# Performance work log

Hardware: AMD Instinct MI355X
Metric: run time of the kernel (lower is better)

## Reference

```python
import jax, jax.numpy as jnp
from jax import lax
import numpy as np

DIM = 768      # model dim
NL = 12        # num mamba layers
DS = 16        # d_state
DI = 1536      # d_inner = 2*dim
DC = 4         # d_conv
P = 16         # patch size
IMG = 256
NP = (IMG // P) ** 2  # 256 patches
GS = 5         # KAN grid_size
SO = 3         # KAN spline_order
NK = NL // 3   # 4 KAN layers
BATCH = 32


def setup_inputs() -> dict:
    key = jax.random.key(0)
    ks = jax.random.split(key, 16)
    def n(k, shape, s=0.02):
        return jax.random.normal(k, shape, jnp.float32) * s
    return {
        "x": jax.random.normal(ks[0], (BATCH, 3, IMG, IMG), jnp.float32),
        "patch_w": n(ks[1], (DIM, 3, P, P)),
        "patch_b": jnp.zeros((DIM,), jnp.float32),
        "pos_embed": n(ks[2], (1, NP, DIM)),
        "in_proj_w": n(ks[3], (NL, 2 * DI, DIM)),
        "conv_w": n(ks[4], (NL, DI, 1, DC), 0.1),
        "conv_b": jnp.zeros((NL, DI), jnp.float32),
        "x_proj_w": n(ks[5], (NL, 2 * DS, DI)),
        "dt_proj_w": n(ks[6], (NL, DS, DI)),
        "dt_proj_b": jnp.zeros((NL, DS), jnp.float32),
        "A_log": jnp.tile(jnp.log(jnp.arange(1, DS + 1, dtype=jnp.float32)), (NL, 1)),
        "D_param": jnp.ones((NL, DI), jnp.float32),
        "out_proj_w": n(ks[7], (NL, DIM, DI)),
        "kan_base_w": n(ks[8], (NK, DIM, DIM)),
        "kan_coeff": n(ks[9], (NK, DIM, DIM, GS + SO), 0.1),
        "kan_bias": n(ks[10], (NK, DIM), 0.01),
        "norm_w": jnp.ones((DIM,), jnp.float32),
        "norm_b": jnp.zeros((DIM,), jnp.float32),
    }


def _mamba_block(x, in_w, cw, cb, xpw, dtw, dtb, alog, Dp, ow):
    Bsz, L, _ = x.shape
    xr = jnp.einsum('bld,ed->ble', x, in_w)              # [B,L,2*DI]
    x1, res = xr[..., :DI], xr[..., DI:]
    # causal depthwise conv (pad d_conv-1 on left, truncate to L)
    xc = lax.conv_general_dilated(
        x1.transpose(0, 2, 1), cw, (1,), [(DC - 1, 0)],
        feature_group_count=DI,
        dimension_numbers=('NCH', 'OIH', 'NCH')) + cb[None, :, None]
    x1 = jax.nn.silu(xc.transpose(0, 2, 1))              # [B,L,DI]
    x_dbl = jnp.einsum('bld,ed->ble', x1, xpw)           # [B,L,2*DS]
    Bp = x_dbl[..., DS:]                                 # dt half of x_proj is discarded (as in torch)
    dt = jax.nn.softplus(jnp.einsum('bld,nd->bln', x1, dtw) + dtb)  # [B,L,DS]
    A = -jnp.exp(alog)                                   # [DS]
    Ad = jnp.exp(A * dt)                                 # [B,L,DS]
    u = x1[..., :DI // DS].mean(-1)                      # [B,L]
    Bd = dt * Bp * u[..., None]                          # [B,L,DS]
    def step(s, ab):
        a, b = ab
        s = s * a + b
        return s, s
    _, ys = lax.scan(step, jnp.zeros((Bsz, DS), x.dtype),
                     (Ad.transpose(1, 0, 2), Bd.transpose(1, 0, 2)))
    y = ys.transpose(1, 0, 2)                            # [B,L,DS]
    y = jnp.repeat(y, DI // DS, axis=-1)                 # n -> (n d)
    y = y + x1 * Dp
    y = y * jax.nn.silu(res)
    return jnp.einsum('bld,ed->ble', y, ow)              # [B,L,DIM]


def _kan(xf, bw, coeff, bias):
    base = xf @ bw.T + bias
    grid = jnp.linspace(-1.0, 1.0, GS + 1)
    denom = grid[1:] - grid[:-1] + 1e-8
    xs = (xf[..., None] - grid[:-1]) / denom             # [M,DIM,GS]
    basis = jnp.where((xs >= 0) & (xs < 1), xs, 0.0)
    return base + jnp.einsum('bik,oik->bo', basis, coeff[:, :, :GS])


def reference(x, patch_w, patch_b, pos_embed, in_proj_w, conv_w, conv_b,
              x_proj_w, dt_proj_w, dt_proj_b, A_log, D_param, out_proj_w,
              kan_base_w, kan_coeff, kan_bias, norm_w, norm_b):
    Bsz = x.shape[0]
    h = lax.conv_general_dilated(
        x, patch_w, (P, P), 'VALID',
        dimension_numbers=('NCHW', 'OIHW', 'NCHW')) + patch_b[None, :, None, None]
    h = h.transpose(0, 2, 3, 1).reshape(Bsz, NP, DIM) + pos_embed
    for i in range(NL):
        h = _mamba_block(h, in_proj_w[i], conv_w[i], conv_b[i], x_proj_w[i],
                         dt_proj_w[i], dt_proj_b[i], A_log[i], D_param[i], out_proj_w[i])
        if i % 3 == 2 and i // 3 < NK:
            j = i // 3
            hf = h.reshape(-1, DIM)
            h = _kan(hf, kan_base_w[j], kan_coeff[j], kan_bias[j]).reshape(Bsz, NP, DIM) + h
    mu = h.mean(-1, keepdims=True)
    var = ((h - mu) ** 2).mean(-1, keepdims=True)
    return (h - mu) / jnp.sqrt(var + 1e-5) * norm_w + norm_b
```

## Files before the change

### kernel.cpp

```cpp
#include <hip/hip_runtime.h>

#define BATCH 32
#define NPATCH 256
#define MROWS (BATCH * NPATCH)
#define DIM 768
#define DI 1536
#define DS 16

typedef __bf16 bf16_t;
typedef __attribute__((ext_vector_type(8))) __bf16 bf16x8;
typedef __attribute__((ext_vector_type(4))) float floatx4;

__device__ __forceinline__ float bf2f(unsigned short u) {
    union { unsigned int i; float f; } v; v.i = ((unsigned int)u) << 16; return v.f;
}
__device__ __forceinline__ unsigned short f2bf(float f) {
    union { float f; unsigned int i; } u; u.f = f;
    unsigned int r = u.i + 0x7FFFu + ((u.i >> 16) & 1u);
    return (unsigned short)(r >> 16);
}
__device__ __forceinline__ float ldin(const void* p, int i, int bf) {
    if (bf) return bf2f(((const unsigned short*)p)[i]);
    return ((const float*)p)[i];
}
__device__ __forceinline__ float4 ldin4(const void* p, int i, int bf) {
    if (bf) {
        ushort4 u = *(const ushort4*)((const unsigned short*)p + i);
        return make_float4(bf2f(u.x), bf2f(u.y), bf2f(u.z), bf2f(u.w));
    }
    return *(const float4*)((const float*)p + i);
}
__device__ __forceinline__ float siluf(float x) { return x / (1.0f + expf(-x)); }

__global__ void detect_k(const void* alog, int* flag) {
    if (threadIdx.x == 0 && blockIdx.x == 0) {
        float v = ((const float*)alog)[1];
        flag[0] = (fabsf(v - 0.69314718f) < 0.01f) ? 0 : 1;
    }
}

__global__ __launch_bounds__(256) void cvt4_k(const int* __restrict__ flag,
                                              const void* __restrict__ in,
                                              unsigned short* __restrict__ out, int n4) {
    int i = blockIdx.x * 256 + threadIdx.x;
    if (i >= n4) return;
    float4 v = ldin4(in, i * 4, flag[0]);
    ushort4 o;
    o.x = f2bf(v.x); o.y = f2bf(v.y); o.z = f2bf(v.z); o.w = f2bf(v.w);
    *(ushort4*)(out + i * 4) = o;
}

__global__ __launch_bounds__(256) void kcoef_k(const int* __restrict__ flag,
                                               const void* __restrict__ co,
                                               bf16_t* __restrict__ out) {
    int idx = blockIdx.x * 256 + threadIdx.x;
    int bf = flag[0];
    int j = idx / (768 * 3840);
    int r = idx - j * (768 * 3840);
    int n = r / 3840;
    int kk = r - n * 3840;
    int i = kk / 5, k5 = kk - i * 5;
    out[idx] = (bf16_t)ldin(co, ((j * 768 + n) * 768 + i) * 8 + k5, bf);
}

__global__ __launch_bounds__(256) void wproj_k(const int* __restrict__ flag,
                                               const void* __restrict__ dtw,
                                               const void* __restrict__ xpw,
                                               bf16_t* __restrict__ w2) {
    int idx = blockIdx.x * 256 + threadIdx.x;
    int bf = flag[0];
    int i = idx / (128 * 1536);
    int r = idx - i * (128 * 1536);
    int n = r / 1536, k = r - n * 1536;
    float v;
    if (n < 16)       v = ldin(dtw, (i * 16 + n) * 1536 + k, bf);
    else if (n < 32)  v = ldin(xpw, (i * 32 + n) * 1536 + k, bf);
    else if (n == 32) v = (k < 96) ? (1.0f / 96.0f) : 0.0f;
    else              v = 0.0f;
    w2[idx] = (bf16_t)v;
}

__global__ __launch_bounds__(256) void cvtconv_k(const int* __restrict__ flag,
                                                 const void* __restrict__ cw,
                                                 bf16_t* __restrict__ cwr) {
    int idx = blockIdx.x * 256 + threadIdx.x;
    int bf = flag[0];
    int i = idx / (4 * 1536);
    int r = idx - i * (4 * 1536);
    int k = r / 1536, c = r - k * 1536;
    cwr[idx] = (bf16_t)ldin(cw, i * 1536 * 4 + c * 4 + k, bf);
}

__global__ __launch_bounds__(256) void basis_k(const bf16_t* __restrict__ h,
                                               bf16_t* __restrict__ bas) {
    int idx = blockIdx.x * 256 + threadIdx.x;
    int m = idx / 96, i8 = (idx - m * 96) * 8;
    bf16x8 hv = *(const bf16x8*)(h + (size_t)m * 768 + i8);
    union { bf16_t a[40]; bf16x8 v[5]; } ob;
#pragma unroll
    for (int ii = 0; ii < 8; ii++) {
        float xv = (float)hv[ii];
#pragma unroll
        for (int k5 = 0; k5 < 5; k5++) {
            float tt = (xv + 1.0f - 0.4f * (float)k5) * 2.5f;
            ob.a[ii * 5 + k5] = (bf16_t)((tt >= 0.0f && tt < 1.0f) ? tt : 0.0f);
        }
    }
    bf16_t* op = bas + (size_t)m * 3840 + (size_t)i8 * 5;
#pragma unroll
    for (int j = 0; j < 5; j++) *(bf16x8*)(op + j * 8) = ob.v[j];
}

__global__ __launch_bounds__(256) void im2col_k(const int* __restrict__ flag,
                                                const void* __restrict__ x,
                                                bf16_t* __restrict__ xp) {
    int idx = blockIdx.x * 256 + threadIdx.x;
    int bf = flag[0];
    int m = idx / 768, kc = idx - m * 768;
    int b = m >> 8, p = m & 255;
    int py = p >> 4, px = p & 15;
    int c = kc >> 8, rr = kc & 255;
    int ky = rr >> 4, kx = rr & 15;
    int src = ((b * 3 + c) * 256 + py * 16 + ky) * 256 + px * 16 + kx;
    xp[idx] = (bf16_t)ldin(x, src, bf);
}

__global__ __launch_bounds__(256) void mgemm_k(
    const bf16_t* __restrict__ A, int lda,
    const bf16_t* __restrict__ W, int ldw,
    bf16_t* __restrict__ C, int ldc,
    int K, int mode, int gx,
    const int* __restrict__ flag,
    const void* __restrict__ bias, int boff,
    const void* __restrict__ aux, int aoff,
    const bf16_t* __restrict__ H, int ldh,
    float* __restrict__ adbd,
    const void* __restrict__ alog, int alo) {
    __shared__ bf16_t sA[128 * 64];
    __shared__ bf16_t sB[128 * 64];
    const int t = threadIdx.x;
    const int lane = t & 63, wave = t >> 6;
    const int wm = wave >> 1, wn = wave & 1;

    const int bid = blockIdx.x;
    const int xcd = bid & 7, l = bid >> 3;
    const int lg = l / gx;
    const int mt = xcd * 8 + lg;
    const int nt = l - lg * gx;
    const int m0 = mt << 7, n0 = nt << 7;

    const int srow = t >> 3;
    const int colperm = (((t & 7) ^ (srow & 7)) << 3);
    const bf16_t* gA[4]; const bf16_t* gB[4];
    char* lA[4]; char* lB[4];
#pragma unroll
    for (int r = 0; r < 4; r++) {
        gA[r] = A + (size_t)(m0 + r * 32 + srow) * lda + colperm;
        gB[r] = W + (size_t)(n0 + r * 32 + srow) * ldw + colperm;
        lA[r] = (char*)sA + (size_t)(r * 256 + wave * 64) * 16;
        lB[r] = (char*)sB + (size_t)(r * 256 + wave * 64) * 16;
    }

    floatx4 acc[4][4];
#pragma unroll
    for (int i = 0; i < 4; i++)
#pragma unroll
        for (int j = 0; j < 4; j++) acc[i][j] = (floatx4){0.f, 0.f, 0.f, 0.f};

    const int kq = lane >> 4;
    const int mr = lane & 15;

    for (int kt = 0; kt < K; kt += 64) {
#pragma unroll
        for (int r = 0; r < 4; r++) {
            __builtin_amdgcn_global_load_lds(
                (__attribute__((address_space(1))) const unsigned int*)(gA[r] + kt),
                (__attribute__((address_space(3))) unsigned int*)lA[r], 16, 0, 0);
            __builtin_amdgcn_global_load_lds(
                (__attribute__((address_space(1))) const unsigned int*)(gB[r] + kt),
                (__attribute__((address_space(3))) unsigned int*)lB[r], 16, 0, 0);
        }
        __syncthreads();
#pragma unroll
        for (int half = 0; half < 2; half++) {
            const int cb = half * 4 + kq;
            bf16x8 af[4], bw[4];
#pragma unroll
            for (int i = 0; i < 4; i++) {
                int rw = wm * 64 + i * 16 + mr;
                af[i] = *(const bf16x8*)(sA + rw * 64 + ((cb ^ (rw & 7)) << 3));
            }
#pragma unroll
            for (int j = 0; j < 4; j++) {
                int rw = wn * 64 + j * 16 + mr;
                bw[j] = *(const bf16x8*)(sB + rw * 64 + ((cb ^ (rw & 7)) << 3));
            }
#pragma unroll
            for (int i = 0; i < 4; i++)
#pragma unroll
                for (int j = 0; j < 4; j++)
                    acc[i][j] = __builtin_amdgcn_mfma_f32_16x16x32_bf16(af[i], bw[j], acc[i][j], 0, 0, 0);
        }
        __syncthreads();
    }

    const int col = lane & 15;
    const int rq = (lane >> 4) * 4;
    const int bff = (mode == 1 || mode == 2 || mode == 4) ? flag[0] : 0;

    if (mode == 4) {
        if (wn == 0) {
            float dtbv = ldin(bias, boff + col, bff);
            float Av = -expf(ldin(alog, alo + col, bff));
#pragma unroll
            for (int i = 0; i < 4; i++) {
#pragma unroll
                for (int reg = 0; reg < 4; reg++) {
                    int gm = m0 + wm * 64 + i * 16 + rq + reg;
                    float uu = __shfl(acc[i][2][reg], (lane & 48));
                    float xdt = acc[i][0][reg] + dtbv;
                    float dt = (xdt > 20.0f) ? xdt : log1pf(expf(xdt));
                    adbd[(size_t)gm * 32 + col] = expf(Av * dt);
                    adbd[(size_t)gm * 32 + 16 + col] = dt * acc[i][1][reg] * uu;
                }
            }
        }
        return;
    }

#pragma unroll
    for (int i = 0; i < 4; i++) {
#pragma unroll
        for (int reg = 0; reg < 4; reg++) {
            int gm = m0 + wm * 64 + i * 16 + rq + reg;
#pragma unroll
            for (int j = 0; j < 4; j++) {
                int gn = n0 + wn * 64 + j * 16 + col;
                float v = acc[i][j][reg];
                if (mode == 1) v += ldin(bias, boff + gn, bff) + ldin(aux, aoff + (gm & 255) * 768 + gn, bff);
                else if (mode == 2) v += ldin(bias, boff + gn, bff);
                else if (mode == 3) v += (float)C[(size_t)gm * ldc + gn] + (float)H[(size_t)gm * ldh + gn];
                C[(size_t)gm * ldc + gn] = (bf16_t)v;
            }
        }
    }
}

__global__ __launch_bounds__(256) void conv_k(const int* __restrict__ flag,
                                              const bf16_t* __restrict__ xr,
                                              const bf16_t* __restrict__ cwr,
                                              const void* __restrict__ cb, int cbo,
                                              bf16_t* __restrict__ xc) {
    int idx = blockIdx.x * 256 + threadIdx.x;
    int bf = flag[0];
    int m = idx / 192, c8 = (idx - m * 192) * 8;
    int l = m & 255;
    float acc[8];
    float4 b0 = ldin4(cb, cbo + c8, bf), b1 = ldin4(cb, cbo + c8 + 4, bf);
    acc[0] = b0.x; acc[1] = b0.y; acc[2] = b0.z; acc[3] = b0.w;
    acc[4] = b1.x; acc[5] = b1.y; acc[6] = b1.z; acc[7] = b1.w;
#pragma unroll
    for (int k = 0; k < 4; k++) {
        if (l + k - 3 >= 0) {
            bf16x8 xv = *(const bf16x8*)(xr + (size_t)(m + k - 3) * 3072 + c8);
            bf16x8 wv = *(const bf16x8*)(cwr + k * 1536 + c8);
#pragma unroll
            for (int j = 0; j < 8; j++) acc[j] += (float)xv[j] * (float)wv[j];
        }
    }
    bf16x8 o;
#pragma unroll
    for (int j = 0; j < 8; j++) o[j] = (bf16_t)siluf(acc[j]);
    *(bf16x8*)(xc + (size_t)m * 1536 + c8) = o;
}

__global__ __launch_bounds__(256) void scan_k(const float* __restrict__ adbd,
                                              float* __restrict__ ys) {
    int wid = (blockIdx.x * 256 + threadIdx.x) >> 6;
    int lane = threadIdx.x & 63;
    int b = wid >> 4, s = wid & 15;
    const float* p = adbd + (size_t)b * (256 * 32);
    float* yo = ys + (size_t)b * (256 * 16);
    float Aj[4], Bj[4];
    float A = 1.0f, Bv = 0.0f;
#pragma unroll
    for (int j = 0; j < 4; j++) {
        int l = lane * 4 + j;
        float a = p[l * 32 + s];
        float bb = p[l * 32 + 16 + s];
        Bv = Bv * a + bb;
        A = A * a;
        Aj[j] = A; Bj[j] = Bv;
    }
#pragma unroll
    for (int off = 1; off < 64; off <<= 1) {
        float pa = __shfl_up(A, off);
        float pb = __shfl_up(Bv, off);
        if (lane >= off) { Bv = pb * A + Bv; A = pa * A; }
    }
    float ex = __shfl_up(Bv, 1);
    if (lane == 0) ex = 0.0f;
#pragma unroll
    for (int j = 0; j < 4; j++) {
        int l = lane * 4 + j;
        yo[l * 16 + s] = Aj[j] * ex + Bj[j];
    }
}

__global__ __launch_bounds__(256) void gate_k(const int* __restrict__ flag,
                                              const float* __restrict__ ys,
                                              bf16_t* __restrict__ xc,
                                              const bf16_t* __restrict__ xr,
                                              const void* __restrict__ Dp, int dpo) {
    int idx = blockIdx.x * 256 + threadIdx.x;
    int bf = flag[0];
    int m = idx / 192, d8 = (idx - m * 192) * 8;
    float yv = ys[m * 16 + d8 / 96];
    bf16x8 rv = *(const bf16x8*)(xr + (size_t)m * 3072 + 1536 + d8);
    bf16x8 xv = *(const bf16x8*)(xc + (size_t)m * 1536 + d8);
    float4 dp0 = ldin4(Dp, dpo + d8, bf), dp1 = ldin4(Dp, dpo + d8 + 4, bf);
    float dpv[8] = {dp0.x, dp0.y, dp0.z, dp0.w, dp1.x, dp1.y, dp1.z, dp1.w};
    bf16x8 o;
#pragma unroll
    for (int j = 0; j < 8; j++) {
        float v = yv + (float)xv[j] * dpv[j];
        o[j] = (bf16_t)(v * siluf((float)rv[j]));
    }
    *(bf16x8*)(xc + (size_t)m * 1536 + d8) = o;
}

__global__ __launch_bounds__(256) void lnorm_k(const int* __restrict__ flag,
                                               const bf16_t* __restrict__ h,
                                               const void* __restrict__ nw,
                                               const void* __restrict__ nb,
                                               void* __restrict__ out) {
    __shared__ float ls[4];
    int bf = flag[0];
    int m = blockIdx.x, t = threadIdx.x;
    const bf16_t* row = h + (size_t)m * 768;
    float v0 = (float)row[t], v1 = (float)row[t + 256], v2 = (float)row[t + 512];
    float s = v0 + v1 + v2;
#pragma unroll
    for (int o = 32; o; o >>= 1) s += __shfl_xor(s, o);
    if ((t & 63) == 0) ls[t >> 6] = s;
    __syncthreads();
    float mu = (ls[0] + ls[1] + ls[2] + ls[3]) * (1.0f / 768.0f);
    __syncthreads();
    float d0 = v0 - mu, d1 = v1 - mu, d2 = v2 - mu;
    float q = d0 * d0 + d1 * d1 + d2 * d2;
#pragma unroll
    for (int o = 32; o; o >>= 1) q += __shfl_xor(q, o);
    if ((t & 63) == 0) ls[t >> 6] = q;
    __syncthreads();
    float var = (ls[0] + ls[1] + ls[2] + ls[3]) * (1.0f / 768.0f);
    float inv = rsqrtf(var + 1e-5f);
    float vv[3] = {d0, d1, d2};
#pragma unroll
    for (int j = 0; j < 3; j++) {
        int colx = t + 256 * j;
        float o = vv[j] * inv * ldin(nw, colx, bf) + ldin(nb, colx, bf);
        size_t oi = (size_t)m * 768 + colx;
        if (bf) ((unsigned short*)out)[oi] = f2bf(o);
        else    ((float*)out)[oi] = o;
    }
}

extern "C" void kernel_launch(void* const* d_in, const int* in_sizes, int n_in,
                              void* d_out, int out_size, void* d_ws, size_t ws_size,
                              hipStream_t stream) {
    const void* x        = d_in[0];
    const void* patch_w  = d_in[1];
    const void* patch_b  = d_in[2];
    const void* pos      = d_in[3];
    const void* in_w     = d_in[4];
    const void* conv_w   = d_in[5];
    const void* conv_b   = d_in[6];
    const void* xpw      = d_in[7];
    const void* dtw      = d_in[8];
    const void* dtb      = d_in[9];
    const void* alog     = d_in[10];
    const void* Dp       = d_in[11];
    const void* out_w    = d_in[12];
    const void* kbw      = d_in[13];
    const void* kcoef    = d_in[14];
    const void* kbias    = d_in[15];
    const void* nw       = d_in[16];
    const void* nb       = d_in[17];

    char* base = (char*)d_ws;
    size_t off = 0;
    int* flag = (int*)base;                          off += 256;
    float* adbd = (float*)(base + off);              off += (size_t)MROWS * 32 * 4;
    float* ysb  = (float*)(base + off);              off += (size_t)MROWS * 16 * 4;
    bf16_t* hA  = (bf16_t*)(base + off);             off += (size_t)MROWS * DIM * 2;
    bf16_t* hB  = (bf16_t*)(base + off);             off += (size_t)MROWS * DIM * 2;
    bf16_t* xr  = (bf16_t*)(base + off);             off += (size_t)MROWS * 2 * DI * 2;
    bf16_t* xc  = (bf16_t*)(base + off);             off += (size_t)MROWS * DI * 2;
    bf16_t* wpatch = (bf16_t*)(base + off);          off += (size_t)DIM * DIM * 2;
    bf16_t* win  = (bf16_t*)(base + off);            off += (size_t)12 * 2 * DI * DIM * 2;
    bf16_t* wout = (bf16_t*)(base + off);            off += (size_t)12 * DIM * DI * 2;
    bf16_t* wkbw = (bf16_t*)(base + off);            off += (size_t)4 * DIM * DIM * 2;
    bf16_t* wkco = (bf16_t*)(base + off);            off += (size_t)4 * DIM * 3840 * 2;
    bf16_t* w2   = (bf16_t*)(base + off);            off += (size_t)12 * 128 * DI * 2;
    bf16_t* cwr  = (bf16_t*)(base + off);            off += (size_t)12 * 4 * DI * 2;
    bf16_t* basis = xr;
    bf16_t* im2c  = xr;

    detect_k<<<1, 64, 0, stream>>>(alog, flag);

    cvt4_k<<<(DIM * DIM / 4 + 255) / 256, 256, 0, stream>>>(flag, patch_w, (unsigned short*)wpatch, DIM * DIM / 4);
    cvt4_k<<<(12 * 2 * DI * DIM / 4 + 255) / 256, 256, 0, stream>>>(flag, in_w, (unsigned short*)win, 12 * 2 * DI * DIM / 4);
    cvt4_k<<<(12 * DIM * DI / 4 + 255) / 256, 256, 0, stream>>>(flag, out_w, (unsigned short*)wout, 12 * DIM * DI / 4);
    cvt4_k<<<(4 * DIM * DIM / 4 + 255) / 256, 256, 0, stream>>>(flag, kbw, (unsigned short*)wkbw, 4 * DIM * DIM / 4);
    kcoef_k<<<4 * DIM * 3840 / 256, 256, 0, stream>>>(flag, kcoef, wkco);
    wproj_k<<<12 * 128 * DI / 256, 256, 0, stream>>>(flag, dtw, xpw, w2);
    cvtconv_k<<<12 * 4 * DI / 256, 256, 0, stream>>>(flag, conv_w, cwr);

    im2col_k<<<(MROWS * DIM) / 256, 256, 0, stream>>>(flag, x, im2c);
    mgemm_k<<<6 * 64, 256, 0, stream>>>(
        im2c, DIM, wpatch, DIM, hA, DIM, DIM, 1, 6,
        flag, patch_b, 0, pos, 0, nullptr, 0, nullptr, nullptr, 0);

    bf16_t* hcur = hA;
    bf16_t* hoth = hB;
    for (int i = 0; i < 12; i++) {
        mgemm_k<<<24 * 64, 256, 0, stream>>>(
            hcur, DIM, win + (size_t)i * 2 * DI * DIM, DIM, xr, 2 * DI, DIM, 0, 24,
            flag, nullptr, 0, nullptr, 0, nullptr, 0, nullptr, nullptr, 0);
        conv_k<<<(MROWS * 192) / 256, 256, 0, stream>>>(
            flag, xr, cwr + (size_t)i * 4 * DI, conv_b, i * DI, xc);
        mgemm_k<<<1 * 64, 256, 0, stream>>>(
            xc, DI, w2 + (size_t)i * 128 * DI, DI, hcur , 128, DI, 4, 1,
            flag, dtb, i * DS, nullptr, 0, nullptr, 0, adbd, alog, i * DS);
        scan_k<<<128, 256, 0, stream>>>(adbd, ysb);
        gate_k<<<(MROWS * 192) / 256, 256, 0, stream>>>(
            flag, ysb, xc, xr, Dp, i * DI);
        mgemm_k<<<6 * 64, 256, 0, stream>>>(
            xc, DI, wout + (size_t)i * DIM * DI, DI, hcur, DIM, DI, 0, 6,
            flag, nullptr, 0, nullptr, 0, nullptr, 0, nullptr, nullptr, 0);
        if (i % 3 == 2) {
            int j = i / 3;
            mgemm_k<<<6 * 64, 256, 0, stream>>>(
                hcur, DIM, wkbw + (size_t)j * DIM * DIM, DIM, hoth, DIM, DIM, 2, 6,
                flag, kbias, j * DIM, nullptr, 0, nullptr, 0, nullptr, nullptr, 0);
            basis_k<<<(MROWS * 96) / 256, 256, 0, stream>>>(hcur, basis);
            mgemm_k<<<6 * 64, 256, 0, stream>>>(
                basis, 3840, wkco + (size_t)j * DIM * 3840, 3840, hoth, DIM, 3840, 3, 6,
                flag, nullptr, 0, nullptr, 0, hcur, DIM, nullptr, nullptr, 0);
            bf16_t* tmp = hcur; hcur = hoth; hoth = tmp;
        }
    }

    lnorm_k<<<MROWS, 256, 0, stream>>>(flag, hcur, nw, nb, d_out);
}
```

Before: 3.087 ms.

## Split-K the small x_proj/dt GEMM with atomics and move dt math into scan

Result: faster. 2.802 ms (-9.2%).

```diff
diff --git a/kernel.cpp b/kernel.cpp
--- a/kernel.cpp
+++ b/kernel.cpp
@@ -134,20 +134,30 @@
     const void* __restrict__ bias, int boff,
     const void* __restrict__ aux, int aoff,
     const bf16_t* __restrict__ H, int ldh,
-    float* __restrict__ adbd,
-    const void* __restrict__ alog, int alo) {
+    float* __restrict__ dtu) {
     __shared__ bf16_t sA[128 * 64];
     __shared__ bf16_t sB[128 * 64];
     const int t = threadIdx.x;
     const int lane = t & 63, wave = t >> 6;
     const int wm = wave >> 1, wn = wave & 1;
 
-    const int bid = blockIdx.x;
-    const int xcd = bid & 7, l = bid >> 3;
-    const int lg = l / gx;
-    const int mt = xcd * 8 + lg;
-    const int nt = l - lg * gx;
-    const int m0 = mt << 7, n0 = nt << 7;
+    int m0, n0, kbeg, kend;
+    if (mode == 5) {
+        int mt = blockIdx.x >> 2, ks = blockIdx.x & 3;
+        m0 = mt << 7; n0 = 0;
+        int KS = K >> 2;
+        kbeg = ks * KS; kend = kbeg + KS;
+    } else {
+        const int bid = blockIdx.x;
+        const int xcd = bid & 7, l = bid >> 3;
+        const int w = gx < 8 ? gx : 8;
+        const int cb8 = w * 8;
+        const int ch = l / cb8, rem = l - ch * cb8;
+        const int mi = rem / w, ni = rem - mi * w;
+        m0 = (xcd * 8 + mi) << 7;
+        n0 = (ch * w + ni) << 7;
+        kbeg = 0; kend = K;
+    }
 
     const int srow = t >> 3;
     const int colperm = (((t & 7) ^ (srow & 7)) << 3);
@@ -170,7 +180,7 @@
     const int kq = lane >> 4;
     const int mr = lane & 15;
 
-    for (int kt = 0; kt < K; kt += 64) {
+    for (int kt = kbeg; kt < kend; kt += 64) {
 #pragma unroll
         for (int r = 0; r < 4; r++) {
             __builtin_amdgcn_global_load_lds(
@@ -206,28 +216,27 @@
 
     const int col = lane & 15;
     const int rq = (lane >> 4) * 4;
-    const int bff = (mode == 1 || mode == 2 || mode == 4) ? flag[0] : 0;
-
-    if (mode == 4) {
+
+    if (mode == 5) {
         if (wn == 0) {
-            float dtbv = ldin(bias, boff + col, bff);
-            float Av = -expf(ldin(alog, alo + col, bff));
 #pragma unroll
             for (int i = 0; i < 4; i++) {
 #pragma unroll
                 for (int reg = 0; reg < 4; reg++) {
                     int gm = m0 + wm * 64 + i * 16 + rq + reg;
-                    float uu = __shfl(acc[i][2][reg], (lane & 48));
-                    float xdt = acc[i][0][reg] + dtbv;
-                    float dt = (xdt > 20.0f) ? xdt : log1pf(expf(xdt));
-                    adbd[(size_t)gm * 32 + col] = expf(Av * dt);
-                    adbd[(size_t)gm * 32 + 16 + col] = dt * acc[i][1][reg] * uu;
+#pragma unroll
+                    for (int j = 0; j < 3; j++) {
+                        int gn = j * 16 + col;
+                        if (gn <= 32)
+                            atomicAdd(&dtu[(size_t)gm * 64 + gn], acc[i][j][reg]);
+                    }
                 }
             }
         }
         return;
     }
 
+    const int bff = (mode == 1 || mode == 2) ? flag[0] : 0;
 #pragma unroll
     for (int i = 0; i < 4; i++) {
 #pragma unroll
@@ -274,20 +283,28 @@
     *(bf16x8*)(xc + (size_t)m * 1536 + c8) = o;
 }
 
-__global__ __launch_bounds__(256) void scan_k(const float* __restrict__ adbd,
+__global__ __launch_bounds__(256) void scan_k(const int* __restrict__ flag,
+                                              const float* __restrict__ dtu,
+                                              const void* __restrict__ dtb, int dtbo,
+                                              const void* __restrict__ alog, int alo,
                                               float* __restrict__ ys) {
     int wid = (blockIdx.x * 256 + threadIdx.x) >> 6;
     int lane = threadIdx.x & 63;
     int b = wid >> 4, s = wid & 15;
-    const float* p = adbd + (size_t)b * (256 * 32);
+    int bf = flag[0];
+    float dtbv = ldin(dtb, dtbo + s, bf);
+    float Av = -expf(ldin(alog, alo + s, bf));
+    const float* p = dtu + (size_t)b * (256 * 64);
     float* yo = ys + (size_t)b * (256 * 16);
     float Aj[4], Bj[4];
     float A = 1.0f, Bv = 0.0f;
 #pragma unroll
     for (int j = 0; j < 4; j++) {
         int l = lane * 4 + j;
-        float a = p[l * 32 + s];
-        float bb = p[l * 32 + 16 + s];
+        float raw = p[l * 64 + s] + dtbv;
+        float dt = (raw > 20.0f) ? raw : log1pf(expf(raw));
+        float a = expf(Av * dt);
+        float bb = dt * p[l * 64 + 16 + s] * p[l * 64 + 32];
         Bv = Bv * a + bb;
         A = A * a;
         Aj[j] = A; Bj[j] = Bv;
@@ -390,7 +407,7 @@
     char* base = (char*)d_ws;
     size_t off = 0;
     int* flag = (int*)base;                          off += 256;
-    float* adbd = (float*)(base + off);              off += (size_t)MROWS * 32 * 4;
+    float* dtu  = (float*)(base + off);              off += (size_t)MROWS * 64 * 4;
     float* ysb  = (float*)(base + off);              off += (size_t)MROWS * 16 * 4;
     bf16_t* hA  = (bf16_t*)(base + off);             off += (size_t)MROWS * DIM * 2;
     bf16_t* hB  = (bf16_t*)(base + off);             off += (size_t)MROWS * DIM * 2;
@@ -419,34 +436,35 @@
     im2col_k<<<(MROWS * DIM) / 256, 256, 0, stream>>>(flag, x, im2c);
     mgemm_k<<<6 * 64, 256, 0, stream>>>(
         im2c, DIM, wpatch, DIM, hA, DIM, DIM, 1, 6,
-        flag, patch_b, 0, pos, 0, nullptr, 0, nullptr, nullptr, 0);
+        flag, patch_b, 0, pos, 0, nullptr, 0, nullptr);
 
     bf16_t* hcur = hA;
     bf16_t* hoth = hB;
     for (int i = 0; i < 12; i++) {
         mgemm_k<<<24 * 64, 256, 0, stream>>>(
             hcur, DIM, win + (size_t)i * 2 * DI * DIM, DIM, xr, 2 * DI, DIM, 0, 24,
-            flag, nullptr, 0, nullptr, 0, nullptr, 0, nullptr, nullptr, 0);
+            flag, nullptr, 0, nullptr, 0, nullptr, 0, nullptr);
         conv_k<<<(MROWS * 192) / 256, 256, 0, stream>>>(
             flag, xr, cwr + (size_t)i * 4 * DI, conv_b, i * DI, xc);
-        mgemm_k<<<1 * 64, 256, 0, stream>>>(
-            xc, DI, w2 + (size_t)i * 128 * DI, DI, hcur , 128, DI, 4, 1,
-            flag, dtb, i * DS, nullptr, 0, nullptr, 0, adbd, alog, i * DS);
-        scan_k<<<128, 256, 0, stream>>>(adbd, ysb);
+        hipMemsetAsync(dtu, 0, (size_t)MROWS * 64 * 4, stream);
+        mgemm_k<<<256, 256, 0, stream>>>(
+            xc, DI, w2 + (size_t)i * 128 * DI, DI, nullptr, 128, DI, 5, 1,
+            flag, nullptr, 0, nullptr, 0, nullptr, 0, dtu);
+        scan_k<<<128, 256, 0, stream>>>(flag, dtu, dtb, i * DS, alog, i * DS, ysb);
         gate_k<<<(MROWS * 192) / 256, 256, 0, stream>>>(
             flag, ysb, xc, xr, Dp, i * DI);
         mgemm_k<<<6 * 64, 256, 0, stream>>>(
             xc, DI, wout + (size_t)i * DIM * DI, DI, hcur, DIM, DI, 0, 6,
-            flag, nullptr, 0, nullptr, 0, nullptr, 0, nullptr, nullptr, 0);
+            flag, nullptr, 0, nullptr, 0, nullptr, 0, nullptr);
         if (i % 3 == 2) {
             int j = i / 3;
             mgemm_k<<<6 * 64, 256, 0, stream>>>(
                 hcur, DIM, wkbw + (size_t)j * DIM * DIM, DIM, hoth, DIM, DIM, 2, 6,
-                flag, kbias, j * DIM, nullptr, 0, nullptr, 0, nullptr, nullptr, 0);
+                flag, kbias, j * DIM, nullptr, 0, nullptr, 0, nullptr);
             basis_k<<<(MROWS * 96) / 256, 256, 0, stream>>>(hcur, basis);
             mgemm_k<<<6 * 64, 256, 0, stream>>>(
                 basis, 3840, wkco + (size_t)j * DIM * 3840, 3840, hoth, DIM, 3840, 3, 6,
-                flag, nullptr, 0, nullptr, 0, hcur, DIM, nullptr, nullptr, 0);
+                flag, nullptr, 0, nullptr, 0, hcur, DIM, nullptr);
             bf16_t* tmp = hcur; hcur = hoth; hoth = tmp;
         }
     }
```
